# Kernel tuning notes

Measured on AMD Instinct MI355X. Metric: run time of the kernel, lower is better.

## Reference

```python
import jax, jax.numpy as jnp
import numpy as np

IGNORE = 5
N_CLASS = 5
MAX_VIEWS = 2048
MAX_VIEWS_BG = 4096


def setup_inputs() -> dict:
    key = jax.random.key(0)
    ks = jax.random.split(key, 8)
    B, C, H, W = 8, 512, 128, 128
    HF, WF = 1024, 1024
    feats = jax.random.normal(ks[0], (B, C, H, W), dtype=jnp.float32)
    labels = jax.random.uniform(ks[1], (B, HF, WF, N_CLASS), dtype=jnp.float32)
    predicts = jax.random.randint(ks[2], (B, H, W), 0, N_CLASS).astype(jnp.int32)
    s = 0.02
    w1 = jax.random.normal(ks[3], (512, 512), jnp.float32) * s
    b1 = jnp.zeros((512,), jnp.float32)
    w2 = jax.random.normal(ks[4], (256, 512), jnp.float32) * s
    b2 = jnp.zeros((256,), jnp.float32)
    w3 = jax.random.normal(ks[5], (256, 256), jnp.float32) * s
    b3 = jnp.zeros((256,), jnp.float32)
    return dict(feats=feats, labels=labels, predicts=predicts,
                w1=w1, b1=b1, w2=w2, b2=b2, w3=w3, b3=b3)


def _leaky(x):
    return jnp.where(x >= 0, x, 0.2 * x)


def _proj_head(x, w1, b1, w2, b2, w3, b3):
    # Linear -> LeakyReLU(0.2) -> Linear -> LeakyReLU(0.2) -> Linear, then L2-normalize (dim=1)
    h = _leaky(x @ w1.T + b1)
    h = _leaky(h @ w2.T + b2)
    h = h @ w3.T + b3
    nrm = jnp.maximum(jnp.linalg.norm(h, axis=1, keepdims=True), 1e-12)
    return h / nrm


def _sample_class(y_hat, y, feats0, c, mv):
    """Stratified hard/easy pixel selection for class c, padded to static size mv.
    Deterministic take-first-k replaces torch.randperm for reproducibility."""
    N = y_hat.shape[0]
    hard = (y_hat == c) & (y != c)
    easy = (y_hat == c) & (y == c)
    nh = hard.sum().astype(jnp.int32)
    ne = easy.sum().astype(jnp.int32)
    cnt = nh + ne
    valid = (cnt > 1).astype(jnp.int32)   # classes with <=1 pixel are skipped in the original
    n_sel = jnp.minimum(cnt, mv) * valid
    both = (2 * nh >= n_sel) & (2 * ne >= n_sel)
    hk = jnp.where(both, n_sel // 2,
                   jnp.where(2 * nh >= n_sel, n_sel - ne, nh))
    ek = n_sel - hk
    idx = jnp.arange(N, dtype=jnp.int32)
    hsel = hard & ((jnp.cumsum(hard) - 1) < hk)   # first hk hard pixels
    esel = easy & ((jnp.cumsum(easy) - 1) < ek)   # first ek easy pixels
    # stream-compaction: hard first, then easy, then padding
    sort_key = jnp.where(hsel, idx, jnp.where(esel, idx + N, 2 * N))
    order = jnp.argsort(sort_key)[:mv]            # static slice of size mv
    row_ok = jnp.arange(mv) < n_sel
    X = feats0[order] * row_ok[:, None]           # zero-pad invalid rows
    yc = jnp.where(row_ok, c, IGNORE)
    return X, yc.astype(jnp.int32)


def reference(feats, labels, predicts, w1, b1, w2, b2, w3, b3):
    B, C, H, W = feats.shape
    lab = jnp.argmax(labels, axis=-1)             # [B, HF, WF]
    sh, sw = lab.shape[1] // H, lab.shape[2] // W
    lab_ds = lab[:, ::sh, ::sw]                   # nearest-neighbor downsample (integer factor)
    # original _hard_anchor_sampling returns inside the batch loop -> only image 0 contributes
    y_hat = lab_ds[0].reshape(-1).astype(jnp.int32)
    y = predicts[0].reshape(-1).astype(jnp.int32)
    feats0 = feats[0].transpose(1, 2, 0).reshape(H * W, C)  # NHWC flatten
    Xs, ys = [], []
    for c in range(N_CLASS):                      # static small class loop
        mv = MAX_VIEWS_BG if c == 0 else MAX_VIEWS
        Xc, yc = _sample_class(y_hat, y, feats0, c, mv)
        Xs.append(Xc)
        ys.append(yc)
    X_ = jnp.concatenate(Xs, axis=0)              # [MV_bg + 4*MV, 512]
    y_ = jnp.concatenate(ys, axis=0)
    anchors = _proj_head(X_, w1, b1, w2, b2, w3, b3)
    return anchors, y_
```

## Files before the change

### kernel.cpp

```cpp
#include <hip/hip_runtime.h>

#define HW 16384
#define IGN 5
#define ROWS_TOTAL 12288
#define ANCH_ELEMS (ROWS_TOTAL * 256)

typedef __bf16 bf16x8 __attribute__((ext_vector_type(8)));
typedef float f32x4 __attribute__((ext_vector_type(4)));
typedef unsigned long long ull;

#define GLDS16(g, l)                                                                     \
    __builtin_amdgcn_global_load_lds((__attribute__((address_space(1))) const void*)(g), \
                                     (__attribute__((address_space(3))) void*)(l), 16, 0, 0)

__device__ __forceinline__ int swz_off(int row, int chunk) {
    return row * 64 + ((chunk ^ (row & 7)) * 8);
}

__global__ void prep_kernel(const float* __restrict__ labels, const int* __restrict__ predicts,
                            int* __restrict__ y_hat, ull* __restrict__ maskH,
                            ull* __restrict__ maskE, int* __restrict__ fwd) {
    int p = blockIdx.x * 256 + threadIdx.x;
    int pr = p >> 7, pc = p & 127;
    const float* lp = labels + ((size_t)(pr * 8) * 1024 + (size_t)(pc * 8)) * 5;
    float best = lp[0];
    int bi = 0;
#pragma unroll
    for (int c = 1; c < 5; ++c) {
        float v = lp[c];
        if (v > best) { best = v; bi = c; }
    }
    y_hat[p] = bi;
    if (p < ROWS_TOTAL) fwd[p] = -1;
    int yy = predicts[p];
    int chunk = p >> 6;
    int lane = threadIdx.x & 63;
#pragma unroll
    for (int c = 0; c < 5; ++c) {
        ull mh = __ballot(bi == c && yy != c);
        ull me = __ballot(bi == c && yy == c);
        if (lane == 0) {
            maskH[c * 256 + chunk] = mh;
            maskE[c * 256 + chunk] = me;
        }
    }
}

__global__ void scan_kernel(const ull* __restrict__ maskH, const ull* __restrict__ maskE,
                            int* __restrict__ baseH, int* __restrict__ baseE,
                            int* __restrict__ nsel, int* __restrict__ hkA,
                            int* __restrict__ ekA) {
    int c = threadIdx.x >> 6;
    int lane = threadIdx.x & 63;
    if (c >= 5) return;
    int ph[4], pe[4];
    int sh = 0, se = 0;
#pragma unroll
    for (int k = 0; k < 4; ++k) {
        int ch = lane * 4 + k;
        ph[k] = sh;
        sh += __popcll(maskH[c * 256 + ch]);
        pe[k] = se;
        se += __popcll(maskE[c * 256 + ch]);
    }
    int incH = sh, incE = se;
#pragma unroll
    for (int d = 1; d < 64; d <<= 1) {
        int t = __shfl_up(incH, d);
        if (lane >= d) incH += t;
        t = __shfl_up(incE, d);
        if (lane >= d) incE += t;
    }
    int exH = incH - sh, exE = incE - se;
#pragma unroll
    for (int k = 0; k < 4; ++k) {
        baseH[c * 256 + lane * 4 + k] = exH + ph[k];
        baseE[c * 256 + lane * 4 + k] = exE + pe[k];
    }
    int nh = __shfl(incH, 63), ne = __shfl(incE, 63);
    if (lane == 0) {
        int mv = (c == 0) ? 4096 : 2048;
        int cnt = nh + ne;
        int n_sel = (cnt > 1) ? ((cnt < mv) ? cnt : mv) : 0;
        int hk;
        if ((2 * nh >= n_sel) && (2 * ne >= n_sel)) hk = n_sel >> 1;
        else if (2 * nh >= n_sel) hk = n_sel - ne;
        else hk = nh;
        nsel[c] = n_sel;
        hkA[c] = hk;
        ekA[c] = n_sel - hk;
    }
}

__global__ void write_inv_kernel(const int* __restrict__ y_hat,
                                 const ull* __restrict__ maskH, const ull* __restrict__ maskE,
                                 const int* __restrict__ baseH, const int* __restrict__ baseE,
                                 const int* __restrict__ hkA, const int* __restrict__ ekA,
                                 const int* __restrict__ nsel, int* __restrict__ fwd,
                                 float* __restrict__ out) {
    int p = blockIdx.x * 256 + threadIdx.x;
    int chunk = p >> 6;
    int lane = threadIdx.x & 63;
    int c = y_hat[p];
    ull mh = maskH[c * 256 + chunk];
    ull me = maskE[c * 256 + chunk];
    ull below = (1ull << lane) - 1ull;
    int cls_base = (c == 0) ? 0 : 4096 + (c - 1) * 2048;
    int res = -1;
    if ((mh >> lane) & 1ull) {
        int pos = baseH[c * 256 + chunk] + __popcll(mh & below);
        if (pos < hkA[c]) res = cls_base + pos;
    } else if ((me >> lane) & 1ull) {
        int pos = baseE[c * 256 + chunk] + __popcll(me & below);
        if (pos < ekA[c]) res = cls_base + hkA[c] + pos;
    }
    if (res >= 0) fwd[res] = p;
    if (p < ROWS_TOTAL) {
        int cc, rin;
        if (p < 4096) { cc = 0; rin = p; }
        else { cc = 1 + ((p - 4096) >> 11); rin = (p - 4096) & 2047; }
        out[ANCH_ELEMS + p] = (float)(rin < nsel[cc] ? cc : IGN);
    }
}

__global__ void conv_x_kernel(const float* __restrict__ F, __bf16* __restrict__ Xb) {
    __shared__ float t[32 * 33];
    int pb = blockIdx.x * 32, chb = blockIdx.y * 32;
    int tid = threadIdx.x;
    int il = tid & 31;
    int grp = tid >> 5;
#pragma unroll
    for (int it = 0; it < 4; ++it) {
        int ch = grp + it * 8;
        t[il * 33 + ch] = F[(size_t)(chb + ch) * HW + pb + il];
    }
    __syncthreads();
#pragma unroll
    for (int it = 0; it < 4; ++it) {
        int p = grp + it * 8;
        Xb[(size_t)(pb + p) * 512 + chb + il] = (__bf16)t[p * 33 + il];
    }
}

__global__ void conv_w_kernel(const float* __restrict__ w1, const float* __restrict__ w2,
                              const float* __restrict__ w3, __bf16* __restrict__ w1b,
                              __bf16* __restrict__ w2b, __bf16* __restrict__ w3b) {
    int i = blockIdx.x * 256 + threadIdx.x;
    if (i < 262144) w1b[i] = (__bf16)w1[i];
    else if (i < 393216) w2b[i - 262144] = (__bf16)w2[i - 262144];
    else if (i < 458752) w3b[i - 393216] = (__bf16)w3[i - 393216];
}

__global__ __launch_bounds__(256) void gemm_bt(const __bf16* __restrict__ A,
                                               const int* __restrict__ fwd,
                                               const __bf16* __restrict__ Bw,
                                               const float* __restrict__ bias,
                                               __bf16* __restrict__ C, int N, int K,
                                               int leaky) {
    const int BK = 64;
    __shared__ __bf16 As[64 * 64];
    __shared__ __bf16 Bs[128 * 64];
    int tid = threadIdx.x;
    int lane = tid & 63;
    int wave_base = tid & 0xC0;
    int wave = tid >> 6;
    int wm = (wave >> 1) * 32, wn = (wave & 1) * 64;
    int mb = blockIdx.y * 64, nb = blockIdx.x * 128;
    int l15 = lane & 15, quad = lane >> 4;

    const __bf16* srcA[2];
    const __bf16* srcB[4];
#pragma unroll
    for (int r = 0; r < 2; ++r) {
        int cc = tid + r * 256;
        int row = cc >> 3, ch = cc & 7;
        int g = mb + row;
        int pix = fwd ? fwd[g] : g;
        if (pix < 0) pix = 0;
        srcA[r] = A + (size_t)pix * K + ((ch ^ (row & 7)) * 8);
    }
#pragma unroll
    for (int r = 0; r < 4; ++r) {
        int cc = tid + r * 256;
        int row = cc >> 3, ch = cc & 7;
        srcB[r] = Bw + (size_t)(nb + row) * K + ((ch ^ (row & 7)) * 8);
    }

    f32x4 acc[2][4] = {};

    for (int kt = 0; kt < K; kt += BK) {
#pragma unroll
        for (int r = 0; r < 2; ++r)
            GLDS16(srcA[r] + kt, As + (size_t)(r * 256 + wave_base) * 8);
#pragma unroll
        for (int r = 0; r < 4; ++r)
            GLDS16(srcB[r] + kt, Bs + (size_t)(r * 256 + wave_base) * 8);
        __syncthreads();
#pragma unroll
        for (int kk = 0; kk < 2; ++kk) {
            bf16x8 af[2], bq[4];
#pragma unroll
            for (int i = 0; i < 2; ++i)
                af[i] = *(const bf16x8*)(As + swz_off(wm + i * 16 + l15, quad + kk * 4));
#pragma unroll
            for (int j = 0; j < 4; ++j)
                bq[j] = *(const bf16x8*)(Bs + swz_off(wn + j * 16 + l15, quad + kk * 4));
#pragma unroll
            for (int i = 0; i < 2; ++i)
#pragma unroll
                for (int j = 0; j < 4; ++j)
                    acc[i][j] = __builtin_amdgcn_mfma_f32_16x16x32_bf16(af[i], bq[j], acc[i][j], 0, 0, 0);
        }
        __syncthreads();
    }

#pragma unroll
    for (int i = 0; i < 2; ++i) {
#pragma unroll
        for (int j = 0; j < 4; ++j) {
            int col = nb + wn + j * 16 + l15;
            float bv = bias[col];
#pragma unroll
            for (int r = 0; r < 4; ++r) {
                int row = mb + wm + i * 16 + quad * 4 + r;
                float v = acc[i][j][r] + bv;
                if (leaky) v = (v >= 0.f) ? v : 0.2f * v;
                C[(size_t)row * N + col] = (__bf16)v;
            }
        }
    }
}

__global__ __launch_bounds__(256) void gemm3_norm(const __bf16* __restrict__ A,
                                                  const __bf16* __restrict__ W,
                                                  const float* __restrict__ bias,
                                                  const int* __restrict__ fwd,
                                                  float* __restrict__ out) {
    const int BK = 64, K = 256;
    __shared__ __bf16 As[64 * 64];
    __shared__ __bf16 Bs[256 * 64];
    __shared__ __bf16 lo[64 * 264];
    __shared__ float nrm[64];
    int tid = threadIdx.x;
    int lane = tid & 63, wave = tid >> 6;
    int wave_base = tid & 0xC0;
    int l15 = lane & 15, quad = lane >> 4;
    int mb = blockIdx.x * 64;
    int wn = wave * 64;

    if (tid < 64) nrm[tid] = 0.f;

    const __bf16* srcA[2];
    const __bf16* srcB[8];
#pragma unroll
    for (int r = 0; r < 2; ++r) {
        int cc = tid + r * 256;
        int row = cc >> 3, ch = cc & 7;
        srcA[r] = A + (size_t)(mb + row) * K + ((ch ^ (row & 7)) * 8);
    }
#pragma unroll
    for (int r = 0; r < 8; ++r) {
        int cc = tid + r * 256;
        int row = cc >> 3, ch = cc & 7;
        srcB[r] = W + (size_t)row * K + ((ch ^ (row & 7)) * 8);
    }

    f32x4 acc[4][4] = {};

    for (int kt = 0; kt < K; kt += BK) {
#pragma unroll
        for (int r = 0; r < 2; ++r)
            GLDS16(srcA[r] + kt, As + (size_t)(r * 256 + wave_base) * 8);
#pragma unroll
        for (int r = 0; r < 8; ++r)
            GLDS16(srcB[r] + kt, Bs + (size_t)(r * 256 + wave_base) * 8);
        __syncthreads();
#pragma unroll
        for (int kk = 0; kk < 2; ++kk) {
            bf16x8 af[4], bq[4];
#pragma unroll
            for (int i = 0; i < 4; ++i)
                af[i] = *(const bf16x8*)(As + swz_off(i * 16 + l15, quad + kk * 4));
#pragma unroll
            for (int j = 0; j < 4; ++j)
                bq[j] = *(const bf16x8*)(Bs + swz_off(wn + j * 16 + l15, quad + kk * 4));
#pragma unroll
            for (int i = 0; i < 4; ++i)
#pragma unroll
                for (int j = 0; j < 4; ++j)
                    acc[i][j] = __builtin_amdgcn_mfma_f32_16x16x32_bf16(af[i], bq[j], acc[i][j], 0, 0, 0);
        }
        __syncthreads();
    }

#pragma unroll
    for (int i = 0; i < 4; ++i) {
#pragma unroll
        for (int r = 0; r < 4; ++r) {
            int row = i * 16 + quad * 4 + r;
            float s = 0.f;
#pragma unroll
            for (int j = 0; j < 4; ++j) {
                int col = wn + j * 16 + l15;
                float v = acc[i][j][r] + bias[col];
                lo[row * 264 + col] = (__bf16)v;
                s += v * v;
            }
            atomicAdd(&nrm[row], s);
        }
    }
    __syncthreads();
    if (tid < 64) {
        float f = 1.0f / fmaxf(sqrtf(nrm[tid]), 1e-12f);
        nrm[tid] = (fwd[mb + tid] >= 0) ? f : 0.f;
    }
    __syncthreads();

#pragma unroll 4
    for (int r = 0; r < 64; ++r) {
        out[(size_t)(mb + r) * 256 + tid] = (float)lo[r * 264 + tid] * nrm[r];
    }
}

extern "C" void kernel_launch(void* const* d_in, const int* in_sizes, int n_in,
                              void* d_out, int out_size, void* d_ws, size_t ws_size,
                              hipStream_t stream) {
    const float* feats = (const float*)d_in[0];
    const float* labels = (const float*)d_in[1];
    const int* predicts = (const int*)d_in[2];
    const float* w1 = (const float*)d_in[3];
    const float* b1 = (const float*)d_in[4];
    const float* w2 = (const float*)d_in[5];
    const float* b2 = (const float*)d_in[6];
    const float* w3 = (const float*)d_in[7];
    const float* b3 = (const float*)d_in[8];
    float* out = (float*)d_out;
    char* ws = (char*)d_ws;

    int* y_hat = (int*)(ws + 0);
    int* fwd = (int*)(ws + (64 << 10));
    int* nsel = (int*)(ws + (128 << 10));
    int* hkA = (int*)(ws + (128 << 10) + 64);
    int* ekA = (int*)(ws + (128 << 10) + 128);
    ull* maskH = (ull*)(ws + (136 << 10));
    ull* maskE = (ull*)(ws + (148 << 10));
    int* baseH = (int*)(ws + (160 << 10));
    int* baseE = (int*)(ws + (168 << 10));
    __bf16* w1b = (__bf16*)(ws + (256 << 10));
    __bf16* w2b = (__bf16*)(ws + (768 << 10));
    __bf16* w3b = (__bf16*)(ws + (1024 << 10));
    __bf16* Xb = (__bf16*)(ws + (2ull << 20));
    __bf16* H1 = (__bf16*)(ws + (18ull << 20));
    __bf16* H2 = (__bf16*)(ws + (34ull << 20));

    prep_kernel<<<64, 256, 0, stream>>>(labels, predicts, y_hat, maskH, maskE, fwd);
    scan_kernel<<<1, 320, 0, stream>>>(maskH, maskE, baseH, baseE, nsel, hkA, ekA);
    write_inv_kernel<<<64, 256, 0, stream>>>(y_hat, maskH, maskE, baseH, baseE, hkA, ekA,
                                             nsel, fwd, out);
    conv_x_kernel<<<dim3(512, 16), 256, 0, stream>>>(feats, Xb);
    conv_w_kernel<<<1792, 256, 0, stream>>>(w1, w2, w3, w1b, w2b, w3b);
    gemm_bt<<<dim3(4, 192), 256, 0, stream>>>(Xb, fwd, w1b, b1, H1, 512, 512, 1);
    gemm_bt<<<dim3(2, 192), 256, 0, stream>>>(H1, nullptr, w2b, b2, H2, 256, 512, 1);
    gemm3_norm<<<192, 256, 0, stream>>>(H2, w3b, b3, fwd, out);
}
```

Measured before the change: 428.8 us.

## Fuse conversion and inverse-index kernels into one launch; enlarge GEMM M-tile to 128

Merges the feature transpose/convert, weight conversion, and forward-index write kernels into a single mid_kernel, dispatching work by block index. This removes two kernel launches and the serialization between them. The two gemm_bt GEMMs also move from 64x128 to 128x128 block tiles with a 4x4 MFMA accumulator per wave. That doubles A-tile reuse and halves block count, at the cost of more registers and LDS per block and fewer blocks to fill the CUs.

Result: no change. 429.5 us (+0.2%).

```diff
diff --git a/kernel.cpp b/kernel.cpp
--- a/kernel.cpp
+++ b/kernel.cpp
@@ -92,15 +92,47 @@
     }
 }
 
-__global__ void write_inv_kernel(const int* __restrict__ y_hat,
-                                 const ull* __restrict__ maskH, const ull* __restrict__ maskE,
-                                 const int* __restrict__ baseH, const int* __restrict__ baseE,
-                                 const int* __restrict__ hkA, const int* __restrict__ ekA,
-                                 const int* __restrict__ nsel, int* __restrict__ fwd,
-                                 float* __restrict__ out) {
-    int p = blockIdx.x * 256 + threadIdx.x;
+__global__ void mid_kernel(const float* __restrict__ F, __bf16* __restrict__ Xb,
+                           const float* __restrict__ w1, const float* __restrict__ w2,
+                           const float* __restrict__ w3, __bf16* __restrict__ w1b,
+                           __bf16* __restrict__ w2b, __bf16* __restrict__ w3b,
+                           const int* __restrict__ y_hat, const ull* __restrict__ maskH,
+                           const ull* __restrict__ maskE, const int* __restrict__ baseH,
+                           const int* __restrict__ baseE, const int* __restrict__ hkA,
+                           const int* __restrict__ ekA, const int* __restrict__ nsel,
+                           int* __restrict__ fwd, float* __restrict__ out) {
+    int tid = threadIdx.x;
+    if (blockIdx.y < 16) {
+        __shared__ float t[32 * 33];
+        int pb = blockIdx.x * 32, chb = blockIdx.y * 32;
+        int il = tid & 31;
+        int grp = tid >> 5;
+#pragma unroll
+        for (int it = 0; it < 4; ++it) {
+            int ch = grp + it * 8;
+            t[il * 33 + ch] = F[(size_t)(chb + ch) * HW + pb + il];
+        }
+        __syncthreads();
+#pragma unroll
+        for (int it = 0; it < 4; ++it) {
+            int p = grp + it * 8;
+            Xb[(size_t)(pb + p) * 512 + chb + il] = (__bf16)t[p * 33 + il];
+        }
+        return;
+    }
+    if (blockIdx.x < 448) {
+#pragma unroll
+        for (int r = 0; r < 4; ++r) {
+            int i = (blockIdx.x * 256 + tid) + r * 114688;
+            if (i < 262144) w1b[i] = (__bf16)w1[i];
+            else if (i < 393216) w2b[i - 262144] = (__bf16)w2[i - 262144];
+            else if (i < 458752) w3b[i - 393216] = (__bf16)w3[i - 393216];
+        }
+        return;
+    }
+    int p = (blockIdx.x - 448) * 256 + tid;
     int chunk = p >> 6;
-    int lane = threadIdx.x & 63;
+    int lane = tid & 63;
     int c = y_hat[p];
     ull mh = maskH[c * 256 + chunk];
     ull me = maskE[c * 256 + chunk];
@@ -123,34 +155,6 @@
     }
 }
 
-__global__ void conv_x_kernel(const float* __restrict__ F, __bf16* __restrict__ Xb) {
-    __shared__ float t[32 * 33];
-    int pb = blockIdx.x * 32, chb = blockIdx.y * 32;
-    int tid = threadIdx.x;
-    int il = tid & 31;
-    int grp = tid >> 5;
-#pragma unroll
-    for (int it = 0; it < 4; ++it) {
-        int ch = grp + it * 8;
-        t[il * 33 + ch] = F[(size_t)(chb + ch) * HW + pb + il];
-    }
-    __syncthreads();
-#pragma unroll
-    for (int it = 0; it < 4; ++it) {
-        int p = grp + it * 8;
-        Xb[(size_t)(pb + p) * 512 + chb + il] = (__bf16)t[p * 33 + il];
-    }
-}
-
-__global__ void conv_w_kernel(const float* __restrict__ w1, const float* __restrict__ w2,
-                              const float* __restrict__ w3, __bf16* __restrict__ w1b,
-                              __bf16* __restrict__ w2b, __bf16* __restrict__ w3b) {
-    int i = blockIdx.x * 256 + threadIdx.x;
-    if (i < 262144) w1b[i] = (__bf16)w1[i];
-    else if (i < 393216) w2b[i - 262144] = (__bf16)w2[i - 262144];
-    else if (i < 458752) w3b[i - 393216] = (__bf16)w3[i - 393216];
-}
-
 __global__ __launch_bounds__(256) void gemm_bt(const __bf16* __restrict__ A,
                                                const int* __restrict__ fwd,
                                                const __bf16* __restrict__ Bw,
@@ -158,39 +162,34 @@
                                                __bf16* __restrict__ C, int N, int K,
                                                int leaky) {
     const int BK = 64;
-    __shared__ __bf16 As[64 * 64];
+    __shared__ __bf16 As[128 * 64];
     __shared__ __bf16 Bs[128 * 64];
     int tid = threadIdx.x;
     int lane = tid & 63;
     int wave_base = tid & 0xC0;
     int wave = tid >> 6;
-    int wm = (wave >> 1) * 32, wn = (wave & 1) * 64;
-    int mb = blockIdx.y * 64, nb = blockIdx.x * 128;
+    int wm = (wave >> 1) * 64, wn = (wave & 1) * 64;
+    int mb = blockIdx.y * 128, nb = blockIdx.x * 128;
     int l15 = lane & 15, quad = lane >> 4;
 
-    const __bf16* srcA[2];
+    const __bf16* srcA[4];
     const __bf16* srcB[4];
 #pragma unroll
-    for (int r = 0; r < 2; ++r) {
+    for (int r = 0; r < 4; ++r) {
         int cc = tid + r * 256;
         int row = cc >> 3, ch = cc & 7;
         int g = mb + row;
         int pix = fwd ? fwd[g] : g;
         if (pix < 0) pix = 0;
         srcA[r] = A + (size_t)pix * K + ((ch ^ (row & 7)) * 8);
-    }
-#pragma unroll
-    for (int r = 0; r < 4; ++r) {
-        int cc = tid + r * 256;
-        int row = cc >> 3, ch = cc & 7;
         srcB[r] = Bw + (size_t)(nb + row) * K + ((ch ^ (row & 7)) * 8);
     }
 
-    f32x4 acc[2][4] = {};
+    f32x4 acc[4][4] = {};
 
     for (int kt = 0; kt < K; kt += BK) {
 #pragma unroll
-        for (int r = 0; r < 2; ++r)
+        for (int r = 0; r < 4; ++r)
             GLDS16(srcA[r] + kt, As + (size_t)(r * 256 + wave_base) * 8);
 #pragma unroll
         for (int r = 0; r < 4; ++r)
@@ -198,15 +197,15 @@
         __syncthreads();
 #pragma unroll
         for (int kk = 0; kk < 2; ++kk) {
-            bf16x8 af[2], bq[4];
-#pragma unroll
-            for (int i = 0; i < 2; ++i)
+            bf16x8 af[4], bq[4];
+#pragma unroll
+            for (int i = 0; i < 4; ++i)
                 af[i] = *(const bf16x8*)(As + swz_off(wm + i * 16 + l15, quad + kk * 4));
 #pragma unroll
             for (int j = 0; j < 4; ++j)
                 bq[j] = *(const bf16x8*)(Bs + swz_off(wn + j * 16 + l15, quad + kk * 4));
 #pragma unroll
-            for (int i = 0; i < 2; ++i)
+            for (int i = 0; i < 4; ++i)
 #pragma unroll
                 for (int j = 0; j < 4; ++j)
                     acc[i][j] = __builtin_amdgcn_mfma_f32_16x16x32_bf16(af[i], bq[j], acc[i][j], 0, 0, 0);
@@ -215,7 +214,7 @@
     }
 
 #pragma unroll
-    for (int i = 0; i < 2; ++i) {
+    for (int i = 0; i < 4; ++i) {
 #pragma unroll
         for (int j = 0; j < 4; ++j) {
             int col = nb + wn + j * 16 + l15;
@@ -355,11 +354,10 @@
 
     prep_kernel<<<64, 256, 0, stream>>>(labels, predicts, y_hat, maskH, maskE, fwd);
     scan_kernel<<<1, 320, 0, stream>>>(maskH, maskE, baseH, baseE, nsel, hkA, ekA);
-    write_inv_kernel<<<64, 256, 0, stream>>>(y_hat, maskH, maskE, baseH, baseE, hkA, ekA,
-                                             nsel, fwd, out);
-    conv_x_kernel<<<dim3(512, 16), 256, 0, stream>>>(feats, Xb);
-    conv_w_kernel<<<1792, 256, 0, stream>>>(w1, w2, w3, w1b, w2b, w3b);
-    gemm_bt<<<dim3(4, 192), 256, 0, stream>>>(Xb, fwd, w1b, b1, H1, 512, 512, 1);
-    gemm_bt<<<dim3(2, 192), 256, 0, stream>>>(H1, nullptr, w2b, b2, H2, 256, 512, 1);
+    mid_kernel<<<dim3(512, 17), 256, 0, stream>>>(feats, Xb, w1, w2, w3, w1b, w2b, w3b,
+                                                  y_hat, maskH, maskE, baseH, baseE, hkA,
+                                                  ekA, nsel, fwd, out);
+    gemm_bt<<<dim3(4, 96), 256, 0, stream>>>(Xb, fwd, w1b, b1, H1, 512, 512, 1);
+    gemm_bt<<<dim3(2, 96), 256, 0, stream>>>(H1, nullptr, w2b, b2, H2, 256, 512, 1);
     gemm3_norm<<<192, 256, 0, stream>>>(H2, w3b, b3, fwd, out);
 }
```
